# Optimization experiments

Hardware: AMD Instinct MI355X
Metric: run time of the kernel (lower is better)

The kernel has to match this reference:

```python
import jax, jax.numpy as jnp
import numpy as np

BATCH, D_IN, D_OUT = 2048, 1024, 4096


def setup_inputs() -> dict:
    key = jax.random.key(0)
    kx, kw = jax.random.split(key)
    x = jax.random.normal(kx, (BATCH, D_IN), dtype=jnp.float32)
    W = jax.random.normal(kw, (D_IN, D_OUT), dtype=jnp.float32)  # nn.Parameter init: N(0,1)
    return {"x": x, "W": W}


def reference(x, W):
    # out[b,o] = -1/2 * sum_i (x[b,i] - W[i,o])^2
    # instead of materializing the [B, O, I] broadcast tensor.
    x_sq = jnp.sum(x * x, axis=1, keepdims=True)          # [B, 1]
    w_sq = jnp.sum(W * W, axis=0, keepdims=True)          # [1, O]
    xw = jnp.matmul(x, W)                                  # [B, O] GEMM
    return -0.5 * (x_sq - 2.0 * xw + w_sq)
```

## Files before the change

kernel.cpp:

```cpp
#include <hip/hip_runtime.h>
#include <stdint.h>

#define BATCH 2048
#define DIN   1024
#define DOUT  4096


__device__ __forceinline__ ushort f2bf(float f) {
    uint32_t u = __float_as_uint(f);
    u += 0x7fffu + ((u >> 16) & 1u);
    return (ushort)(u >> 16);
}

__device__ __forceinline__ void async_copy16(const void* gsrc, void* ldst) {
    __builtin_amdgcn_global_load_lds(
        reinterpret_cast<uint32_t __attribute__((address_space(1)))*>(
            reinterpret_cast<uintptr_t>(gsrc)),
        reinterpret_cast<uint32_t __attribute__((address_space(3)))*>(
            reinterpret_cast<uintptr_t>(ldst)),
        16, 0, 0);
}

typedef __bf16 bf16x8 __attribute__((ext_vector_type(8)));
typedef float  f32x4  __attribute__((ext_vector_type(4)));


__global__ __launch_bounds__(256) void prep_x(const float* __restrict__ x,
                                              ushort* __restrict__ xb,
                                              float* __restrict__ xsq) {
    const int row = blockIdx.x;
    const int t = threadIdx.x;
    const float4 v = *(const float4*)(x + (size_t)row * DIN + t * 4);
    ushort4 pk;
    pk.x = f2bf(v.x); pk.y = f2bf(v.y); pk.z = f2bf(v.z); pk.w = f2bf(v.w);
    *(ushort4*)(xb + (size_t)row * DIN + t * 4) = pk;

    float s = v.x * v.x + v.y * v.y + v.z * v.z + v.w * v.w;
    #pragma unroll
    for (int off = 32; off > 0; off >>= 1) s += __shfl_down(s, off);
    __shared__ float ws[4];
    if ((t & 63) == 0) ws[t >> 6] = s;
    __syncthreads();
    if (t == 0) xsq[row] = ws[0] + ws[1] + ws[2] + ws[3];
}

__global__ __launch_bounds__(256) void prep_w(const float* __restrict__ W,
                                              ushort* __restrict__ wbt,
                                              float* __restrict__ wsqp) {
    __shared__ float tile[64][65];
    const int o0 = blockIdx.x * 64;
    const int jb = blockIdx.y;
    const int tx = threadIdx.x & 63;
    const int ty = threadIdx.x >> 6;

    float ssq = 0.f;
    for (int sub = 0; sub < 4; ++sub) {
        const int i0 = jb * 256 + sub * 64;
        if (sub) __syncthreads();
        #pragma unroll
        for (int r = ty; r < 64; r += 4) {
            const float v = W[(size_t)(i0 + r) * DOUT + o0 + tx];
            tile[r][tx] = v;
            ssq += v * v;
        }
        __syncthreads();
        #pragma unroll
        for (int r = ty; r < 64; r += 4)
            wbt[(size_t)(o0 + r) * DIN + i0 + tx] = f2bf(tile[tx][r]);
    }
    __syncthreads();
    tile[ty][tx] = ssq;
    __syncthreads();
    if (ty == 0)
        wsqp[(size_t)jb * DOUT + o0 + tx] =
            tile[0][tx] + tile[1][tx] + tile[2][tx] + tile[3][tx];
}

#define BM 128
#define BN 128
#define BK 32

__global__ __launch_bounds__(256, 2) void gemm_bt_epi(
    const ushort* __restrict__ A,
    const ushort* __restrict__ Bt,
    const float* __restrict__ xsq,
    const float* __restrict__ wsqp,
    float* __restrict__ out) {
    __shared__ __align__(16) ushort sA[BM * BK];
    __shared__ __align__(16) ushort sB[BN * BK];

    const int tid  = threadIdx.x;
    const int wv   = tid >> 6;
    const int lane = tid & 63;
    const int wr = wv >> 1, wc = wv & 1;
    const int m0 = blockIdx.y * BM;
    const int n0 = blockIdx.x * BN;

    const int st_row = wv * 32 + (lane >> 2);
    const int st_col = (((lane & 3) - (lane >> 3)) & 3) * 8;

    const ushort* agp0 = A  + (size_t)(m0 + st_row)      * DIN + st_col;
    const ushort* agp1 = A  + (size_t)(m0 + st_row + 16) * DIN + st_col;
    const ushort* bgp0 = Bt + (size_t)(n0 + st_row)      * DIN + st_col;
    const ushort* bgp1 = Bt + (size_t)(n0 + st_row + 16) * DIN + st_col;

    ushort* sA0 = &sA[wv * 1024];
    ushort* sA1 = &sA[wv * 1024 + 512];
    ushort* sB0 = &sB[wv * 1024];
    ushort* sB1 = &sB[wv * 1024 + 512];

    f32x4 acc[4][4] = {};

    const int a_row = wr * 64 + (lane & 15);
    const int b_row = wc * 64 + (lane & 15);
    const int kp    = ((((lane >> 4) + ((lane & 15) >> 1)) & 3)) * 8;

    for (int kt = 0; kt < DIN; kt += BK) {
        __syncthreads();
        async_copy16(agp0 + kt, sA0);
        async_copy16(agp1 + kt, sA1);
        async_copy16(bgp0 + kt, sB0);
        async_copy16(bgp1 + kt, sB1);
        __syncthreads();

        bf16x8 fa[4], fb[4];
        #pragma unroll
        for (int i = 0; i < 4; ++i)
            fa[i] = *(const bf16x8*)&sA[(a_row + i * 16) * BK + kp];
        #pragma unroll
        for (int i = 0; i < 4; ++i)
            fb[i] = *(const bf16x8*)&sB[(b_row + i * 16) * BK + kp];

        #pragma unroll
        for (int mi = 0; mi < 4; ++mi)
            #pragma unroll
            for (int ni = 0; ni < 4; ++ni)
                acc[mi][ni] = __builtin_amdgcn_mfma_f32_16x16x32_bf16(
                    fa[mi], fb[ni], acc[mi][ni], 0, 0, 0);
    }

    const int er = (lane >> 4) * 4;
    const int ec = lane & 15;
    float wh[4];
    #pragma unroll
    for (int ni = 0; ni < 4; ++ni) {
        const int col = n0 + wc * 64 + ni * 16 + ec;
        wh[ni] = 0.5f * (wsqp[col] + wsqp[DOUT + col] +
                         wsqp[2 * DOUT + col] + wsqp[3 * DOUT + col]);
    }
    #pragma unroll
    for (int mi = 0; mi < 4; ++mi) {
        const int row = m0 + wr * 64 + mi * 16 + er;
        #pragma unroll
        for (int r = 0; r < 4; ++r) {
            const float xh = 0.5f * xsq[row + r];
            #pragma unroll
            for (int ni = 0; ni < 4; ++ni) {
                const int col = n0 + wc * 64 + ni * 16 + ec;
                out[(size_t)(row + r) * DOUT + col] = acc[mi][ni][r] - xh - wh[ni];
            }
        }
    }
}


extern "C" void kernel_launch(void* const* d_in, const int* in_sizes, int n_in,
                              void* d_out, int out_size, void* d_ws, size_t ws_size,
                              hipStream_t stream) {
    const float* x = (const float*)d_in[0];
    const float* W = (const float*)d_in[1];
    float* out = (float*)d_out;

    char* ws = (char*)d_ws;
    ushort* xb   = (ushort*)ws;
    ushort* wbt  = (ushort*)(ws + (4u << 20));
    float*  xsq  = (float*)(ws + (12u << 20));
    float*  wsqp = (float*)(ws + (12u << 20) + (32u << 10));

    prep_x<<<BATCH, 256, 0, stream>>>(x, xb, xsq);
    prep_w<<<dim3(DOUT / 64, 4), 256, 0, stream>>>(W, wbt, wsqp);
    gemm_bt_epi<<<dim3(DOUT / BN, BATCH / BM), 256, 0, stream>>>(xb, wbt, xsq, wsqp, out);
}
```

Before: 121.8 us.

## Fuse x and W prep kernels and double GEMM K-tile with new LDS swizzle

Merges the x-conversion and W-transpose prep kernels into one launch, with block ranges split by role, to save a kernel launch and let the two preps overlap. The GEMM K-tile grows from 32 to 64, so each barrier pair covers twice as many MFMAs, and the async LDS loads and the XOR-style swizzle are rewritten for 8 16-byte chunks per row. LDS use per block doubles to 32KB, which may limit occupancy, and the loads are still not double-buffered.

```diff
diff --git a/kernel.cpp b/kernel.cpp
--- a/kernel.cpp
+++ b/kernel.cpp
@@ -24,61 +24,69 @@
 typedef __bf16 bf16x8 __attribute__((ext_vector_type(8)));
 typedef float  f32x4  __attribute__((ext_vector_type(4)));
 
-
-__global__ __launch_bounds__(256) void prep_x(const float* __restrict__ x,
-                                              ushort* __restrict__ xb,
-                                              float* __restrict__ xsq) {
-    const int row = blockIdx.x;
-    const int t = threadIdx.x;
-    const float4 v = *(const float4*)(x + (size_t)row * DIN + t * 4);
-    ushort4 pk;
-    pk.x = f2bf(v.x); pk.y = f2bf(v.y); pk.z = f2bf(v.z); pk.w = f2bf(v.w);
-    *(ushort4*)(xb + (size_t)row * DIN + t * 4) = pk;
-
-    float s = v.x * v.x + v.y * v.y + v.z * v.z + v.w * v.w;
-    #pragma unroll
-    for (int off = 32; off > 0; off >>= 1) s += __shfl_down(s, off);
-    __shared__ float ws[4];
-    if ((t & 63) == 0) ws[t >> 6] = s;
-    __syncthreads();
-    if (t == 0) xsq[row] = ws[0] + ws[1] + ws[2] + ws[3];
-}
-
-__global__ __launch_bounds__(256) void prep_w(const float* __restrict__ W,
-                                              ushort* __restrict__ wbt,
-                                              float* __restrict__ wsqp) {
+__global__ __launch_bounds__(256) void prep_fused(const float* __restrict__ x,
+                                                  const float* __restrict__ W,
+                                                  ushort* __restrict__ xb,
+                                                  float* __restrict__ xsq,
+                                                  ushort* __restrict__ wbt,
+                                                  float* __restrict__ wsqp) {
     __shared__ float tile[64][65];
-    const int o0 = blockIdx.x * 64;
-    const int jb = blockIdx.y;
-    const int tx = threadIdx.x & 63;
-    const int ty = threadIdx.x >> 6;
-
-    float ssq = 0.f;
-    for (int sub = 0; sub < 4; ++sub) {
-        const int i0 = jb * 256 + sub * 64;
-        if (sub) __syncthreads();
-        #pragma unroll
-        for (int r = ty; r < 64; r += 4) {
-            const float v = W[(size_t)(i0 + r) * DOUT + o0 + tx];
-            tile[r][tx] = v;
-            ssq += v * v;
+    const int b = blockIdx.x;
+    if (b < 256) {
+        const int o0 = (b >> 2) * 64;
+        const int jb = b & 3;
+        const int tx = threadIdx.x & 63;
+        const int ty = threadIdx.x >> 6;
+        float ssq = 0.f;
+        for (int sub = 0; sub < 4; ++sub) {
+            const int i0 = jb * 256 + sub * 64;
+            if (sub) __syncthreads();
+            #pragma unroll
+            for (int r = ty; r < 64; r += 4) {
+                const float v = W[(size_t)(i0 + r) * DOUT + o0 + tx];
+                tile[r][tx] = v;
+                ssq += v * v;
+            }
+            __syncthreads();
+            #pragma unroll
+            for (int r = ty; r < 64; r += 4)
+                wbt[(size_t)(o0 + r) * DIN + i0 + tx] = f2bf(tile[tx][r]);
         }
         __syncthreads();
+        tile[ty][tx] = ssq;
+        __syncthreads();
+        if (ty == 0)
+            wsqp[(size_t)jb * DOUT + o0 + tx] =
+                tile[0][tx] + tile[1][tx] + tile[2][tx] + tile[3][tx];
+    } else {
+        const int blk  = b - 256;
+        const int wv   = threadIdx.x >> 6;
+        const int lane = threadIdx.x & 63;
         #pragma unroll
-        for (int r = ty; r < 64; r += 4)
-            wbt[(size_t)(o0 + r) * DIN + i0 + tx] = f2bf(tile[tx][r]);
+        for (int rr = 0; rr < 4; ++rr) {
+            const int row = blk * 16 + wv * 4 + rr;
+            const float4* src = (const float4*)(x + (size_t)row * DIN);
+            ushort4* dst = (ushort4*)(xb + (size_t)row * DIN);
+            float s = 0.f;
+            #pragma unroll
+            for (int c = 0; c < 4; ++c) {
+                const float4 v = src[c * 64 + lane];
+                ushort4 pk;
+                pk.x = f2bf(v.x); pk.y = f2bf(v.y);
+                pk.z = f2bf(v.z); pk.w = f2bf(v.w);
+                dst[c * 64 + lane] = pk;
+                s += v.x * v.x + v.y * v.y + v.z * v.z + v.w * v.w;
+            }
+            #pragma unroll
+            for (int off = 32; off > 0; off >>= 1) s += __shfl_down(s, off);
+            if (lane == 0) xsq[row] = s;
+        }
     }
-    __syncthreads();
-    tile[ty][tx] = ssq;
-    __syncthreads();
-    if (ty == 0)
-        wsqp[(size_t)jb * DOUT + o0 + tx] =
-            tile[0][tx] + tile[1][tx] + tile[2][tx] + tile[3][tx];
 }
 
 #define BM 128
 #define BN 128
-#define BK 32
+#define BK 64
 
 __global__ __launch_bounds__(256, 2) void gemm_bt_epi(
     const ushort* __restrict__ A,
@@ -96,47 +104,47 @@
     const int m0 = blockIdx.y * BM;
     const int n0 = blockIdx.x * BN;
 
-    const int st_row = wv * 32 + (lane >> 2);
-    const int st_col = (((lane & 3) - (lane >> 3)) & 3) * 8;
+    const int st_row = wv * 32 + (lane >> 3);
+    const int st_c   = ((((lane & 7) - (lane >> 3)) & 7)) * 8;
 
-    const ushort* agp0 = A  + (size_t)(m0 + st_row)      * DIN + st_col;
-    const ushort* agp1 = A  + (size_t)(m0 + st_row + 16) * DIN + st_col;
-    const ushort* bgp0 = Bt + (size_t)(n0 + st_row)      * DIN + st_col;
-    const ushort* bgp1 = Bt + (size_t)(n0 + st_row + 16) * DIN + st_col;
-
-    ushort* sA0 = &sA[wv * 1024];
-    ushort* sA1 = &sA[wv * 1024 + 512];
-    ushort* sB0 = &sB[wv * 1024];
-    ushort* sB1 = &sB[wv * 1024 + 512];
+    const ushort* agp = A  + (size_t)(m0 + st_row) * DIN + st_c;
+    const ushort* bgp = Bt + (size_t)(n0 + st_row) * DIN + st_c;
 
     f32x4 acc[4][4] = {};
 
     const int a_row = wr * 64 + (lane & 15);
     const int b_row = wc * 64 + (lane & 15);
-    const int kp    = ((((lane >> 4) + ((lane & 15) >> 1)) & 3)) * 8;
+    int kpos[2];
+    #pragma unroll
+    for (int kk = 0; kk < 2; ++kk)
+        kpos[kk] = ((((lane >> 4) + 4 * kk + (lane & 7)) & 7)) * 8;
 
     for (int kt = 0; kt < DIN; kt += BK) {
         __syncthreads();
-        async_copy16(agp0 + kt, sA0);
-        async_copy16(agp1 + kt, sA1);
-        async_copy16(bgp0 + kt, sB0);
-        async_copy16(bgp1 + kt, sB1);
+        #pragma unroll
+        for (int q = 0; q < 4; ++q)
+            async_copy16(agp + (size_t)q * 8 * DIN + kt, &sA[wv * 2048 + q * 512]);
+        #pragma unroll
+        for (int q = 0; q < 4; ++q)
+            async_copy16(bgp + (size_t)q * 8 * DIN + kt, &sB[wv * 2048 + q * 512]);
         __syncthreads();
 
-        bf16x8 fa[4], fb[4];
         #pragma unroll
-        for (int i = 0; i < 4; ++i)
-            fa[i] = *(const bf16x8*)&sA[(a_row + i * 16) * BK + kp];
-        #pragma unroll
-        for (int i = 0; i < 4; ++i)
-            fb[i] = *(const bf16x8*)&sB[(b_row + i * 16) * BK + kp];
-
-        #pragma unroll
-        for (int mi = 0; mi < 4; ++mi)
+        for (int kk = 0; kk < 2; ++kk) {
+            bf16x8 fa[4], fb[4];
             #pragma unroll
-            for (int ni = 0; ni < 4; ++ni)
-                acc[mi][ni] = __builtin_amdgcn_mfma_f32_16x16x32_bf16(
-                    fa[mi], fb[ni], acc[mi][ni], 0, 0, 0);
+            for (int i = 0; i < 4; ++i)
+                fa[i] = *(const bf16x8*)&sA[(a_row + i * 16) * BK + kpos[kk]];
+            #pragma unroll
+            for (int i = 0; i < 4; ++i)
+                fb[i] = *(const bf16x8*)&sB[(b_row + i * 16) * BK + kpos[kk]];
+            #pragma unroll
+            for (int mi = 0; mi < 4; ++mi)
+                #pragma unroll
+                for (int ni = 0; ni < 4; ++ni)
+                    acc[mi][ni] = __builtin_amdgcn_mfma_f32_16x16x32_bf16(
+                        fa[mi], fb[ni], acc[mi][ni], 0, 0, 0);
+        }
     }
 
     const int er = (lane >> 4) * 4;
@@ -177,7 +185,6 @@
     float*  xsq  = (float*)(ws + (12u << 20));
     float*  wsqp = (float*)(ws + (12u << 20) + (32u << 10));
 
-    prep_x<<<BATCH, 256, 0, stream>>>(x, xb, xsq);
-    prep_w<<<dim3(DOUT / 64, 4), 256, 0, stream>>>(W, wbt, wsqp);
+    prep_fused<<<384, 256, 0, stream>>>(x, W, xb, xsq, wbt, wsqp);
     gemm_bt_epi<<<dim3(DOUT / BN, BATCH / BM), 256, 0, stream>>>(xb, wbt, xsq, wsqp, out);
 }
```

Result: faster. 114.1 us (-6.3%).
